# Performance work log

Measured on AMD Instinct MI355X. Metric: run time of the kernel, lower is better.

## Reference

```python
import jax, jax.numpy as jnp
import numpy as np

B, N, K, U = 64, 4096, 32, 16
NUM_STEPS = 8
NUM_CLASSES = 2


def setup_inputs() -> dict:
    key = jax.random.key(0)
    ks = jax.random.split(key, 17)
    s = 0.05
    g = lambda k, shape: jax.random.normal(k, shape, dtype=jnp.float32) * s
    return {
        "inputs": jax.random.normal(ks[0], (B, N, K + 2), dtype=jnp.float32),
        # UGRNN cell params
        "Wn": g(ks[1], (K, U)),
        "Wg": g(ks[2], (U, U)), "Ug": g(ks[3], (U, U)), "bg": jnp.zeros((U,), jnp.float32),
        "Wc": g(ks[4], (U, U)), "Uc": g(ks[5], (U, U)), "bc": jnp.zeros((U,), jnp.float32),
        "We": g(ks[6], (U, U)), "be": jnp.zeros((U,), jnp.float32),
        # MLP head (Dropout is identity at inference)
        "W1": g(ks[7], (N * U, 256)), "b1": jnp.zeros((256,), jnp.float32),
        "W2": g(ks[8], (256, 32)),    "b2": jnp.zeros((32,), jnp.float32),
        "W3": g(ks[9], (32, NUM_CLASSES)), "b3": jnp.zeros((NUM_CLASSES,), jnp.float32),
    }


def reference(inputs, Wn, Wg, Ug, bg, Wc, Uc, bc, We, be, W1, b1, W2, b2, W3, b3):
    # split channels: node scalar, K neighbour features, edge scalar
    h0 = inputs[..., 0]            # [B, N]
    neigh = inputs[..., 1:-1]      # [B, N, K]
    e0 = inputs[..., -1]           # [B, N]

    units = Wg.shape[0]
    h = jnp.broadcast_to(h0[..., None], h0.shape + (units,))  # tile -> [B, N, U]
    e = jnp.broadcast_to(e0[..., None], e0.shape + (units,))  # tile -> [B, N, U]

    # neighbour aggregation/projection is constant across steps -> hoist
    m = jnp.einsum("bnk,ku->bnu", neigh, Wn)  # [B, N, U]

    for _ in range(NUM_STEPS):  # small fixed unroll over num_steps
        x = m + e
        g = jax.nn.sigmoid(x @ Wg + h @ Ug + bg)  # update gate
        c = jnp.tanh(x @ Wc + h @ Uc + bc)        # candidate
        h = g * h + (1.0 - g) * c                 # UGRNN update
        e = jnp.tanh(x @ We + be)                 # edge state update

    out = h.reshape(h.shape[0], -1)               # Flatten -> [B, N*U]
    out = jax.nn.relu(out @ W1 + b1)
    out = jax.nn.relu(out @ W2 + b2)
    return jax.nn.softmax(out @ W3 + b3, axis=-1)  # [B, num_classes]
```

## Files before the change

kernel.cpp:

```cpp
#include <hip/hip_runtime.h>
#include <hip/hip_bf16.h>

typedef _Float16 half8_t __attribute__((ext_vector_type(8)));
typedef _Float16 half4_t __attribute__((ext_vector_type(4)));
typedef float    f32x4  __attribute__((ext_vector_type(4)));

#define MFMA32(a, b, c) __builtin_amdgcn_mfma_f32_16x16x32_f16((a), (b), (c), 0, 0, 0)
#define MFMA16(a, b, c) __builtin_amdgcn_mfma_f32_16x16x16f16((a), (b), (c), 0, 0, 0)

__device__ __forceinline__ void load_lds16(const void* g, void* l) {
    __builtin_amdgcn_global_load_lds(
        (const __attribute__((address_space(1))) unsigned int*)g,
        (__attribute__((address_space(3))) unsigned int*)l, 16, 0, 0);
}

__global__
__attribute__((amdgpu_flat_work_group_size(256, 256)))
void ugrnn_mfma(
    const float* __restrict__ inputs,
    const float* __restrict__ Wn, const float* __restrict__ Wg,
    const float* __restrict__ Ug, const float* __restrict__ bg,
    const float* __restrict__ Wc, const float* __restrict__ Uc,
    const float* __restrict__ bc, const float* __restrict__ We,
    const float* __restrict__ be, _Float16* __restrict__ h_t)
{
    __shared__ float raw[4][2 * 544];

    const int wave = threadIdx.x >> 6;
    const int lane = threadIdx.x & 63;
    const int t16  = lane & 15;
    const int q    = lane >> 4;

    const int pair = blockIdx.x * 4 + wave;
    const int b    = pair >> 7;
    const int n0   = (pair & 127) << 5;

    const float* gsrc = inputs + ((size_t)b * 4096 + n0) * 34;
    float* rw = raw[wave];
#pragma unroll
    for (int r = 0; r < 17; ++r) rw[r * 64 + lane] = gsrc[r * 64 + lane];

    half8_t An;
#pragma unroll
    for (int i = 0; i < 8; ++i)
        An[i] = (_Float16)Wn[(q * 8 + i) * 16 + t16];

    half4_t Awg, Aug, Awc, Auc, Awe;
#pragma unroll
    for (int i = 0; i < 4; ++i) {
        const int k = 4 * q + i;
        Awg[i] = (_Float16)Wg[k * 16 + t16];
        Aug[i] = (_Float16)Ug[k * 16 + t16];
        Awc[i] = (_Float16)Wc[k * 16 + t16];
        Auc[i] = (_Float16)Uc[k * 16 + t16];
        Awe[i] = (_Float16)We[k * 16 + t16];
    }
    f32x4 bgC, bcC, beC;
#pragma unroll
    for (int r = 0; r < 4; ++r) {
        bgC[r] = bg[4 * q + r];
        bcC[r] = bc[4 * q + r];
        beC[r] = be[4 * q + r];
    }

    f32x4 m[2], h[2], e[2];
    const f32x4 zc = {0.f, 0.f, 0.f, 0.f};
#pragma unroll
    for (int u2 = 0; u2 < 2; ++u2) {
        const float* rt = rw + u2 * 544;
        half8_t Bx;
#pragma unroll
        for (int i = 0; i < 8; ++i)
            Bx[i] = (_Float16)rt[t16 * 34 + 1 + q * 8 + i];
        m[u2] = MFMA32(An, Bx, zc);
        const float h0 = rt[t16 * 34 + 0];
        const float e0 = rt[t16 * 34 + 33];
        h[u2] = (f32x4){h0, h0, h0, h0};
        e[u2] = (f32x4){e0, e0, e0, e0};
    }

#pragma unroll 1
    for (int step = 0; step < 8; ++step) {
        f32x4 gp[2], cp[2], ep[2];
#pragma unroll
        for (int u2 = 0; u2 < 2; ++u2) {
            const f32x4 x = m[u2] + e[u2];
            half4_t xB, hB;
#pragma unroll
            for (int r = 0; r < 4; ++r) {
                xB[r] = (_Float16)x[r];
                hB[r] = (_Float16)h[u2][r];
            }
            gp[u2] = MFMA16(Aug, hB, MFMA16(Awg, xB, bgC));
            cp[u2] = MFMA16(Auc, hB, MFMA16(Awc, xB, bcC));
            if (step < 7) ep[u2] = MFMA16(Awe, xB, beC);
        }
#pragma unroll
        for (int u2 = 0; u2 < 2; ++u2) {
#pragma unroll
            for (int r = 0; r < 4; ++r) {
                float gv = __builtin_amdgcn_rcpf(1.0f + __expf(-gp[u2][r]));
                float cv = 1.0f - 2.0f * __builtin_amdgcn_rcpf(1.0f + __expf(2.0f * cp[u2][r]));
                h[u2][r] = cv + gv * (h[u2][r] - cv);
                if (step < 7)
                    e[u2][r] = 1.0f - 2.0f * __builtin_amdgcn_rcpf(1.0f + __expf(2.0f * ep[u2][r]));
            }
        }
    }

#pragma unroll
    for (int u2 = 0; u2 < 2; ++u2) {
        half4_t hv;
#pragma unroll
        for (int r = 0; r < 4; ++r) hv[r] = (_Float16)h[u2][r];
        *(half4_t*)(h_t + (size_t)b * 65536
                        + (size_t)(n0 + u2 * 16 + t16) * 16 + 4 * q) = hv;
    }
}

__global__
__attribute__((amdgpu_flat_work_group_size(256, 256), amdgpu_waves_per_eu(1, 2)))
void fc1_mfma(const _Float16* __restrict__ h_t, const float* __restrict__ W1,
              _Float16* __restrict__ partials)
{
    __shared__ float w1s[2][64][258];
    const int tid  = threadIdx.x;
    const int wave = tid >> 6;
    const int lane = tid & 63;
    const int t16  = lane & 15;
    const int q    = lane >> 4;
    const int i0   = blockIdx.x * 256;

    f32x4 acc[4][4];
#pragma unroll
    for (int mt = 0; mt < 4; ++mt)
#pragma unroll
        for (int nt = 0; nt < 4; ++nt)
            acc[mt][nt] = (f32x4){0.f, 0.f, 0.f, 0.f};

#pragma unroll
    for (int r = 0; r < 16; ++r) {
        int row = wave * 16 + r;
        load_lds16(W1 + (size_t)(i0 + row) * 256 + lane * 4, &w1s[0][row][0]);
    }
    __syncthreads();

#pragma unroll 1
    for (int c = 0; c < 4; ++c) {
        const int buf = c & 1;
        const int cb  = i0 + c * 64;

        half8_t A[2][4];
#pragma unroll
        for (int ks = 0; ks < 2; ++ks)
#pragma unroll
            for (int mt = 0; mt < 4; ++mt)
                A[ks][mt] = *(const half8_t*)(h_t
                    + (size_t)(mt * 16 + t16) * 65536 + cb + ks * 32 + q * 8);

        if (c < 3) {
#pragma unroll
            for (int r = 0; r < 16; ++r) {
                int row = wave * 16 + r;
                load_lds16(W1 + (size_t)(cb + 64 + row) * 256 + lane * 4,
                           &w1s[buf ^ 1][row][0]);
            }
        }

#pragma unroll
        for (int ks = 0; ks < 2; ++ks) {
#pragma unroll
            for (int nt = 0; nt < 4; ++nt) {
                int j = (wave * 4 + nt) * 16 + t16;
                half8_t Bf;
#pragma unroll
                for (int i = 0; i < 8; ++i)
                    Bf[i] = (_Float16)w1s[buf][ks * 32 + q * 8 + i][j];
#pragma unroll
                for (int mt = 0; mt < 4; ++mt)
                    acc[mt][nt] = MFMA32(A[ks][mt], Bf, acc[mt][nt]);
            }
        }
        __syncthreads();
    }

    _Float16* pb = partials + (size_t)blockIdx.x * 16384;
#pragma unroll
    for (int mt = 0; mt < 4; ++mt)
#pragma unroll
        for (int nt = 0; nt < 4; ++nt)
#pragma unroll
            for (int r = 0; r < 4; ++r)
                pb[(mt * 16 + 4 * q + r) * 256 + (wave * 4 + nt) * 16 + t16] =
                    (_Float16)acc[mt][nt][r];
}

__global__ __launch_bounds__(1024) void mlp_tail(
    const _Float16* __restrict__ partials, const float* __restrict__ b1,
    const float* __restrict__ W2, const float* __restrict__ b2,
    const float* __restrict__ W3, const float* __restrict__ b3,
    float* __restrict__ out)
{
    __shared__ float x1p[4][256];
    __shared__ float x1s[256];
    __shared__ float x2q[32][33];
    __shared__ float x2s[32];
    __shared__ float lg[2];
    const int b = blockIdx.x, tid = threadIdx.x;
    const int j = tid & 255, kg = tid >> 8;

    const _Float16* p = partials + (size_t)(kg * 64) * 16384 + (size_t)b * 256 + j;
    float s0 = 0.f, s1 = 0.f, s2 = 0.f, s3 = 0.f;
#pragma unroll 4
    for (int k = 0; k < 64; k += 4) {
        s0 += (float)p[(size_t)(k + 0) * 16384];
        s1 += (float)p[(size_t)(k + 1) * 16384];
        s2 += (float)p[(size_t)(k + 2) * 16384];
        s3 += (float)p[(size_t)(k + 3) * 16384];
    }
    x1p[kg][j] = s0 + s1 + s2 + s3;
    __syncthreads();
    if (tid < 256)
        x1s[j] = fmaxf(b1[j] + x1p[0][j] + x1p[1][j] + x1p[2][j] + x1p[3][j], 0.f);
    __syncthreads();

    const int j2 = tid & 31, g2 = tid >> 5;
    float s = 0.f;
#pragma unroll
    for (int k = g2 * 8; k < g2 * 8 + 8; ++k) s += x1s[k] * W2[k * 32 + j2];
    x2q[g2][j2] = s;
    __syncthreads();
    if (tid < 32) {
        float t = b2[tid];
#pragma unroll
        for (int g = 0; g < 32; ++g) t += x2q[g][tid];
        x2s[tid] = fmaxf(t, 0.f);
    }
    __syncthreads();
    if (tid < 2) {
        float t = b3[tid];
#pragma unroll
        for (int k = 0; k < 32; ++k) t += x2s[k] * W3[k * 2 + tid];
        lg[tid] = t;
    }
    __syncthreads();
    if (tid == 0) {
        float mx = fmaxf(lg[0], lg[1]);
        float e0 = __expf(lg[0] - mx), e1 = __expf(lg[1] - mx);
        float inv = 1.0f / (e0 + e1);
        out[b * 2 + 0] = e0 * inv;
        out[b * 2 + 1] = e1 * inv;
    }
}

extern "C" void kernel_launch(void* const* d_in, const int* in_sizes, int n_in,
                              void* d_out, int out_size, void* d_ws, size_t ws_size,
                              hipStream_t stream) {
    const float* inputs = (const float*)d_in[0];
    const float* Wn = (const float*)d_in[1];
    const float* Wg = (const float*)d_in[2];
    const float* Ug = (const float*)d_in[3];
    const float* bg = (const float*)d_in[4];
    const float* Wc = (const float*)d_in[5];
    const float* Uc = (const float*)d_in[6];
    const float* bc = (const float*)d_in[7];
    const float* We = (const float*)d_in[8];
    const float* be = (const float*)d_in[9];
    const float* W1 = (const float*)d_in[10];
    const float* b1 = (const float*)d_in[11];
    const float* W2 = (const float*)d_in[12];
    const float* b2 = (const float*)d_in[13];
    const float* W3 = (const float*)d_in[14];
    const float* b3 = (const float*)d_in[15];
    float* out = (float*)d_out;

    _Float16* h_t      = (_Float16*)d_ws;
    _Float16* partials = (_Float16*)((char*)d_ws + (size_t)64 * 65536 * 2);

    ugrnn_mfma<<<2048, 256, 0, stream>>>(inputs, Wn, Wg, Ug, bg, Wc, Uc, bc,
                                         We, be, h_t);
    fc1_mfma<<<256, 256, 0, stream>>>(h_t, W1, partials);
    mlp_tail<<<64, 1024, 0, stream>>>(partials, b1, W2, b2, W3, b3, out);
}
```

Baseline: 182.9 us.

## Double-buffer UGRNN inputs, fold exp scaling into weights, widen fc1 blocks

The UGRNN kernel now makes each wave process two 32-node tiles. The second tile's inputs are prefetched into LDS via global_load_lds while the first tile's recurrence runs, and the grid is halved. The log2(e) scaling is folded into the gate weights so the code uses exp2 directly, and the three reciprocals per element are merged into one shared rcp. Conversions use packed cvt_pkrtz, and fc1 moves to 512-thread blocks with half the N-tiles per wave. The tail reduction reads half4 vectors across 16 k-groups. The merged reciprocal can overflow when the exponent terms are large, and round-toward-zero conversion shifts accuracy slightly.

```diff
diff --git a/kernel.cpp b/kernel.cpp
--- a/kernel.cpp
+++ b/kernel.cpp
@@ -1,8 +1,8 @@
 #include <hip/hip_runtime.h>
-#include <hip/hip_bf16.h>
 
 typedef _Float16 half8_t __attribute__((ext_vector_type(8)));
 typedef _Float16 half4_t __attribute__((ext_vector_type(4)));
+typedef __fp16   fp16x2  __attribute__((ext_vector_type(2)));
 typedef float    f32x4  __attribute__((ext_vector_type(4)));
 
 #define MFMA32(a, b, c) __builtin_amdgcn_mfma_f32_16x16x32_f16((a), (b), (c), 0, 0, 0)
@@ -12,6 +12,20 @@
     __builtin_amdgcn_global_load_lds(
         (const __attribute__((address_space(1))) unsigned int*)g,
         (__attribute__((address_space(3))) unsigned int*)l, 16, 0, 0);
+}
+__device__ __forceinline__ void load_lds4(const void* g, void* l) {
+    __builtin_amdgcn_global_load_lds(
+        (const __attribute__((address_space(1))) unsigned int*)g,
+        (__attribute__((address_space(3))) unsigned int*)l, 4, 0, 0);
+}
+
+__device__ __forceinline__ half4_t pk4(f32x4 v) {
+    fp16x2 lo = __builtin_amdgcn_cvt_pkrtz(v[0], v[1]);
+    fp16x2 hi = __builtin_amdgcn_cvt_pkrtz(v[2], v[3]);
+    half4_t r;
+    r[0] = (_Float16)lo[0]; r[1] = (_Float16)lo[1];
+    r[2] = (_Float16)hi[0]; r[3] = (_Float16)hi[1];
+    return r;
 }
 
 __global__
@@ -24,21 +38,18 @@
     const float* __restrict__ bc, const float* __restrict__ We,
     const float* __restrict__ be, _Float16* __restrict__ h_t)
 {
-    __shared__ float raw[4][2 * 544];
+    __shared__ float raw[4][2][1088];
 
     const int wave = threadIdx.x >> 6;
     const int lane = threadIdx.x & 63;
     const int t16  = lane & 15;
     const int q    = lane >> 4;
 
-    const int pair = blockIdx.x * 4 + wave;
-    const int b    = pair >> 7;
-    const int n0   = (pair & 127) << 5;
-
-    const float* gsrc = inputs + ((size_t)b * 4096 + n0) * 34;
-    float* rw = raw[wave];
-#pragma unroll
-    for (int r = 0; r < 17; ++r) rw[r * 64 + lane] = gsrc[r * 64 + lane];
+    const int pidx0 = blockIdx.x * 4 + wave;
+    const int pidx1 = pidx0 + 4096;
+
+    const float NL2E = -1.44269504f;
+    const float TL2E =  2.88539008f;
 
     half8_t An;
 #pragma unroll
@@ -49,77 +60,114 @@
 #pragma unroll
     for (int i = 0; i < 4; ++i) {
         const int k = 4 * q + i;
-        Awg[i] = (_Float16)Wg[k * 16 + t16];
-        Aug[i] = (_Float16)Ug[k * 16 + t16];
-        Awc[i] = (_Float16)Wc[k * 16 + t16];
-        Auc[i] = (_Float16)Uc[k * 16 + t16];
-        Awe[i] = (_Float16)We[k * 16 + t16];
+        Awg[i] = (_Float16)(Wg[k * 16 + t16] * NL2E);
+        Aug[i] = (_Float16)(Ug[k * 16 + t16] * NL2E);
+        Awc[i] = (_Float16)(Wc[k * 16 + t16] * TL2E);
+        Auc[i] = (_Float16)(Uc[k * 16 + t16] * TL2E);
+        Awe[i] = (_Float16)(We[k * 16 + t16] * TL2E);
     }
     f32x4 bgC, bcC, beC;
 #pragma unroll
     for (int r = 0; r < 4; ++r) {
-        bgC[r] = bg[4 * q + r];
-        bcC[r] = bc[4 * q + r];
-        beC[r] = be[4 * q + r];
-    }
-
-    f32x4 m[2], h[2], e[2];
+        bgC[r] = bg[4 * q + r] * NL2E;
+        bcC[r] = bc[4 * q + r] * TL2E;
+        beC[r] = be[4 * q + r] * TL2E;
+    }
+
+    const float* g0 = inputs + (size_t)pidx0 * 1088;
+    const float* g1 = inputs + (size_t)pidx1 * 1088;
+    float* buf0 = &raw[wave][0][0];
+    float* buf1 = &raw[wave][1][0];
+
+    f32x4 m0[2], h0a[2], e0a[2], m1[2], h1a[2], e1a[2];
     const f32x4 zc = {0.f, 0.f, 0.f, 0.f};
-#pragma unroll
-    for (int u2 = 0; u2 < 2; ++u2) {
-        const float* rt = rw + u2 * 544;
-        half8_t Bx;
-#pragma unroll
-        for (int i = 0; i < 8; ++i)
-            Bx[i] = (_Float16)rt[t16 * 34 + 1 + q * 8 + i];
-        m[u2] = MFMA32(An, Bx, zc);
-        const float h0 = rt[t16 * 34 + 0];
-        const float e0 = rt[t16 * 34 + 33];
-        h[u2] = (f32x4){h0, h0, h0, h0};
-        e[u2] = (f32x4){e0, e0, e0, e0};
-    }
-
+
+    auto init_pair = [&](const float* rt, f32x4* m, f32x4* h, f32x4* e) {
+#pragma unroll
+        for (int u2 = 0; u2 < 2; ++u2) {
+            const float* rp = rt + u2 * 544;
+            half8_t Bx;
+#pragma unroll
+            for (int i = 0; i < 8; ++i)
+                Bx[i] = (_Float16)rp[t16 * 34 + 1 + q * 8 + i];
+            m[u2] = MFMA32(An, Bx, zc);
+            const float hv = rp[t16 * 34 + 0];
+            const float ev = rp[t16 * 34 + 33];
+            h[u2] = (f32x4){hv, hv, hv, hv};
+            e[u2] = (f32x4){ev, ev, ev, ev};
+        }
+    };
+
+    auto run_pair = [&](int pidx, f32x4* m, f32x4* h, f32x4* e) {
 #pragma unroll 1
-    for (int step = 0; step < 8; ++step) {
-        f32x4 gp[2], cp[2], ep[2];
-#pragma unroll
-        for (int u2 = 0; u2 < 2; ++u2) {
-            const f32x4 x = m[u2] + e[u2];
-            half4_t xB, hB;
-#pragma unroll
-            for (int r = 0; r < 4; ++r) {
-                xB[r] = (_Float16)x[r];
-                hB[r] = (_Float16)h[u2][r];
+        for (int step = 0; step < 8; ++step) {
+            f32x4 gp[2], cp[2], ep[2];
+#pragma unroll
+            for (int u2 = 0; u2 < 2; ++u2) {
+                const f32x4 x = m[u2] + e[u2];
+                half4_t xB = pk4(x);
+                half4_t hB = pk4(h[u2]);
+                gp[u2] = MFMA16(Aug, hB, MFMA16(Awg, xB, bgC));
+                cp[u2] = MFMA16(Auc, hB, MFMA16(Awc, xB, bcC));
+                if (step < 7) ep[u2] = MFMA16(Awe, xB, beC);
             }
-            gp[u2] = MFMA16(Aug, hB, MFMA16(Awg, xB, bgC));
-            cp[u2] = MFMA16(Auc, hB, MFMA16(Awc, xB, bcC));
-            if (step < 7) ep[u2] = MFMA16(Awe, xB, beC);
-        }
-#pragma unroll
-        for (int u2 = 0; u2 < 2; ++u2) {
-#pragma unroll
-            for (int r = 0; r < 4; ++r) {
-                float gv = __builtin_amdgcn_rcpf(1.0f + __expf(-gp[u2][r]));
-                float cv = 1.0f - 2.0f * __builtin_amdgcn_rcpf(1.0f + __expf(2.0f * cp[u2][r]));
-                h[u2][r] = cv + gv * (h[u2][r] - cv);
-                if (step < 7)
-                    e[u2][r] = 1.0f - 2.0f * __builtin_amdgcn_rcpf(1.0f + __expf(2.0f * ep[u2][r]));
+#pragma unroll
+            for (int u2 = 0; u2 < 2; ++u2) {
+#pragma unroll
+                for (int r = 0; r < 4; ++r) {
+                    const float Ae = 1.0f + __builtin_amdgcn_exp2f(gp[u2][r]);
+                    const float Be = 1.0f + __builtin_amdgcn_exp2f(cp[u2][r]);
+                    if (step < 7) {
+                        const float Ce = 1.0f + __builtin_amdgcn_exp2f(ep[u2][r]);
+                        const float BC = Be * Ce;
+                        const float rr = __builtin_amdgcn_rcpf(Ae * BC);
+                        const float gv = rr * BC;
+                        const float rb = rr * (Ae * Ce);
+                        const float rc = rr * (Ae * Be);
+                        const float cv = 1.0f - 2.0f * rb;
+                        h[u2][r] = cv + gv * (h[u2][r] - cv);
+                        e[u2][r] = 1.0f - 2.0f * rc;
+                    } else {
+                        const float rr = __builtin_amdgcn_rcpf(Ae * Be);
+                        const float gv = rr * Be;
+                        const float cv = 1.0f - 2.0f * (rr * Ae);
+                        h[u2][r] = cv + gv * (h[u2][r] - cv);
+                    }
+                }
             }
         }
-    }
-
-#pragma unroll
-    for (int u2 = 0; u2 < 2; ++u2) {
-        half4_t hv;
-#pragma unroll
-        for (int r = 0; r < 4; ++r) hv[r] = (_Float16)h[u2][r];
-        *(half4_t*)(h_t + (size_t)b * 65536
-                        + (size_t)(n0 + u2 * 16 + t16) * 16 + 4 * q) = hv;
-    }
+        const int b  = pidx >> 7;
+        const int n0 = (pidx & 127) << 5;
+#pragma unroll
+        for (int u2 = 0; u2 < 2; ++u2)
+            *(half4_t*)(h_t + (size_t)b * 65536
+                            + (size_t)(n0 + u2 * 16 + t16) * 16 + 4 * q) =
+                pk4(h[u2]);
+    };
+
+#pragma unroll
+    for (int k2 = 0; k2 < 4; ++k2)
+        load_lds16(g0 + k2 * 256 + lane * 4, buf0 + k2 * 256);
+    load_lds4(g0 + 1024 + lane, buf0 + 1024);
+    asm volatile("s_waitcnt vmcnt(0)" ::: "memory");
+    __builtin_amdgcn_sched_barrier(0);
+    init_pair(buf0, m0, h0a, e0a);
+
+#pragma unroll
+    for (int k2 = 0; k2 < 4; ++k2)
+        load_lds16(g1 + k2 * 256 + lane * 4, buf1 + k2 * 256);
+    load_lds4(g1 + 1024 + lane, buf1 + 1024);
+
+    run_pair(pidx0, m0, h0a, e0a);
+
+    asm volatile("s_waitcnt vmcnt(0)" ::: "memory");
+    __builtin_amdgcn_sched_barrier(0);
+    init_pair(buf1, m1, h1a, e1a);
+    run_pair(pidx1, m1, h1a, e1a);
 }
 
 __global__
-__attribute__((amdgpu_flat_work_group_size(256, 256), amdgpu_waves_per_eu(1, 2)))
+__attribute__((amdgpu_flat_work_group_size(512, 512), amdgpu_waves_per_eu(1, 2)))
 void fc1_mfma(const _Float16* __restrict__ h_t, const float* __restrict__ W1,
               _Float16* __restrict__ partials)
 {
@@ -131,16 +179,16 @@
     const int q    = lane >> 4;
     const int i0   = blockIdx.x * 256;
 
-    f32x4 acc[4][4];
+    f32x4 acc[4][2];
 #pragma unroll
     for (int mt = 0; mt < 4; ++mt)
 #pragma unroll
-        for (int nt = 0; nt < 4; ++nt)
+        for (int nt = 0; nt < 2; ++nt)
             acc[mt][nt] = (f32x4){0.f, 0.f, 0.f, 0.f};
 
 #pragma unroll
-    for (int r = 0; r < 16; ++r) {
-        int row = wave * 16 + r;
+    for (int r = 0; r < 8; ++r) {
+        int row = wave * 8 + r;
         load_lds16(W1 + (size_t)(i0 + row) * 256 + lane * 4, &w1s[0][row][0]);
     }
     __syncthreads();
@@ -160,8 +208,8 @@
 
         if (c < 3) {
 #pragma unroll
-            for (int r = 0; r < 16; ++r) {
-                int row = wave * 16 + r;
+            for (int r = 0; r < 8; ++r) {
+                int row = wave * 8 + r;
                 load_lds16(W1 + (size_t)(cb + 64 + row) * 256 + lane * 4,
                            &w1s[buf ^ 1][row][0]);
             }
@@ -170,8 +218,8 @@
 #pragma unroll
         for (int ks = 0; ks < 2; ++ks) {
 #pragma unroll
-            for (int nt = 0; nt < 4; ++nt) {
-                int j = (wave * 4 + nt) * 16 + t16;
+            for (int nt = 0; nt < 2; ++nt) {
+                int j = (wave * 2 + nt) * 16 + t16;
                 half8_t Bf;
 #pragma unroll
                 for (int i = 0; i < 8; ++i)
@@ -188,10 +236,10 @@
 #pragma unroll
     for (int mt = 0; mt < 4; ++mt)
 #pragma unroll
-        for (int nt = 0; nt < 4; ++nt)
+        for (int nt = 0; nt < 2; ++nt)
 #pragma unroll
             for (int r = 0; r < 4; ++r)
-                pb[(mt * 16 + 4 * q + r) * 256 + (wave * 4 + nt) * 16 + t16] =
+                pb[(mt * 16 + 4 * q + r) * 256 + (wave * 2 + nt) * 16 + t16] =
                     (_Float16)acc[mt][nt][r];
 }
 
@@ -201,27 +249,34 @@
     const float* __restrict__ W3, const float* __restrict__ b3,
     float* __restrict__ out)
 {
-    __shared__ float x1p[4][256];
+    __shared__ float x1p[16][256];
     __shared__ float x1s[256];
     __shared__ float x2q[32][33];
     __shared__ float x2s[32];
     __shared__ float lg[2];
     const int b = blockIdx.x, tid = threadIdx.x;
-    const int j = tid & 255, kg = tid >> 8;
-
-    const _Float16* p = partials + (size_t)(kg * 64) * 16384 + (size_t)b * 256 + j;
+    const int kg = tid >> 6, l64 = tid & 63;
+    const int j0 = l64 * 4;
+
+    const _Float16* p = partials + (size_t)(kg * 16) * 16384 + (size_t)b * 256 + j0;
     float s0 = 0.f, s1 = 0.f, s2 = 0.f, s3 = 0.f;
-#pragma unroll 4
-    for (int k = 0; k < 64; k += 4) {
-        s0 += (float)p[(size_t)(k + 0) * 16384];
-        s1 += (float)p[(size_t)(k + 1) * 16384];
-        s2 += (float)p[(size_t)(k + 2) * 16384];
-        s3 += (float)p[(size_t)(k + 3) * 16384];
-    }
-    x1p[kg][j] = s0 + s1 + s2 + s3;
-    __syncthreads();
-    if (tid < 256)
-        x1s[j] = fmaxf(b1[j] + x1p[0][j] + x1p[1][j] + x1p[2][j] + x1p[3][j], 0.f);
+#pragma unroll
+    for (int k = 0; k < 16; ++k) {
+        half4_t v = *(const half4_t*)(p + (size_t)k * 16384);
+        s0 += (float)v[0]; s1 += (float)v[1]; s2 += (float)v[2]; s3 += (float)v[3];
+    }
+    x1p[kg][j0 + 0] = s0;
+    x1p[kg][j0 + 1] = s1;
+    x1p[kg][j0 + 2] = s2;
+    x1p[kg][j0 + 3] = s3;
+    __syncthreads();
+
+    if (tid < 256) {
+        float t = b1[tid];
+#pragma unroll
+        for (int g = 0; g < 16; ++g) t += x1p[g][tid];
+        x1s[tid] = fmaxf(t, 0.f);
+    }
     __syncthreads();
 
     const int j2 = tid & 31, g2 = tid >> 5;
@@ -277,8 +332,8 @@
     _Float16* h_t      = (_Float16*)d_ws;
     _Float16* partials = (_Float16*)((char*)d_ws + (size_t)64 * 65536 * 2);
 
-    ugrnn_mfma<<<2048, 256, 0, stream>>>(inputs, Wn, Wg, Ug, bg, Wc, Uc, bc,
+    ugrnn_mfma<<<1024, 256, 0, stream>>>(inputs, Wn, Wg, Ug, bg, Wc, Uc, bc,
                                          We, be, h_t);
-    fc1_mfma<<<256, 256, 0, stream>>>(h_t, W1, partials);
+    fc1_mfma<<<256, 512, 0, stream>>>(h_t, W1, partials);
     mlp_tail<<<64, 1024, 0, stream>>>(partials, b1, W2, b2, W3, b3, out);
 }
```

Result: slower. 188.6 us (+3.2%).
